# Kernel tuning notes

Hardware: AMD Instinct MI355X
Metric: run time of the kernel (lower is better)

Reference implementation:

```python
import jax, jax.numpy as jnp
import numpy as np

B, S, I = 64, 32, 64
N_ITEMS = 100000
E, H = 256, 128


def setup_inputs() -> dict:
    key = jax.random.key(0)
    k_len, k_ids, k_ut, k_emb, k_wih, k_whh, k_a1, k_a2, k_vt = jax.random.split(key, 9)
    n_sess = B * S
    # ragged session lengths in [2, I] -> trailing zero padding, all sessions valid
    lengths = jax.random.randint(k_len, (n_sess,), 2, I + 1)
    ids = jax.random.randint(k_ids, (n_sess, I), 1, N_ITEMS + 1)
    pad_mask = jnp.arange(I)[None, :] < lengths[:, None]
    item_id = (ids * pad_mask).reshape(B, S, I).astype(jnp.int32)
    eval_from = jnp.zeros((B,), dtype=jnp.int32)
    u_type = jax.random.randint(k_ut, (B,), 0, 5).astype(jnp.int32)
    sc = 0.05
    emb = jax.random.normal(k_emb, (N_ITEMS + 1, E), jnp.float32) * sc
    emb = emb.at[0].set(0.0)  # padding_idx=0
    W_ih = jax.random.normal(k_wih, (3 * H, E), jnp.float32) * sc
    W_hh = jax.random.normal(k_whh, (3 * H, H), jnp.float32) * sc
    b_ih = jnp.zeros((3 * H,), jnp.float32)
    b_hh = jnp.zeros((3 * H,), jnp.float32)
    W_a1 = jax.random.normal(k_a1, (H, H), jnp.float32) * sc
    W_a2 = jax.random.normal(k_a2, (H, H), jnp.float32) * sc
    W_vt = jax.random.normal(k_vt, (1, H), jnp.float32) * sc
    return {"item_id": item_id, "eval_from": eval_from, "u_type": u_type,
            "emb": emb, "W_ih": W_ih, "W_hh": W_hh, "b_ih": b_ih, "b_hh": b_hh,
            "W_a1": W_a1, "W_a2": W_a2, "W_vt": W_vt}


def _gru(x, lengths, W_ih, W_hh, b_ih, b_hh):
    # x: [L, N, E]; packed-GRU semantics: state frozen past each length,
    # outputs zero at padded steps (matches pad_packed_sequence).
    L, N, _ = x.shape
    Hh = W_hh.shape[1]

    def step(h, inp):
        xt, t = inp
        gi = xt @ W_ih.T + b_ih           # [N, 3H]
        gh = h @ W_hh.T + b_hh
        i_r, i_z, i_n = jnp.split(gi, 3, axis=-1)
        h_r, h_z, h_n = jnp.split(gh, 3, axis=-1)
        r = jax.nn.sigmoid(i_r + h_r)
        z = jax.nn.sigmoid(i_z + h_z)
        n = jnp.tanh(i_n + r * h_n)
        h_new = (1.0 - z) * n + z * h
        valid = (t < lengths)[:, None]
        h_next = jnp.where(valid, h_new, h)
        out = jnp.where(valid, h_new, 0.0)
        return h_next, out

    h0 = jnp.zeros((N, Hh), x.dtype)
    hT, outs = jax.lax.scan(step, h0, (x, jnp.arange(L)))
    return outs, hT  # outs: [L, N, H], hT: [N, H]


def reference(item_id, eval_from, u_type, emb, W_ih, W_hh, b_ih, b_hh, W_a1, W_a2, W_vt):
    b, s, i = item_id.shape
    ids = jnp.clip(item_id, 0)
    allow = jnp.arange(s)[None, :] >= eval_from[:, None]        # [B, S]
    ids = ids * allow[:, :, None].astype(ids.dtype)
    sess = ids.reshape(b * s, i)                                # [N, I]
    lengths = (sess != 0).sum(1)                                # all >= 2 by construction
    n = sess.shape[0]
    target = sess[jnp.arange(n), lengths - 1]
    len_in = lengths - 1
    L = i - 1  # static L_in_max; extra padded steps are masked out
    mask = (jnp.arange(L)[None, :] < len_in[:, None])           # [N, L]
    inp = sess[:, :L] * mask.astype(sess.dtype)
    x = emb[inp]                                                # [N, L, E] (dropout=identity, eval)
    outs, ht = _gru(x.transpose(1, 0, 2), len_in, W_ih, W_hh, b_ih, b_hh)
    gru = outs.transpose(1, 0, 2)                               # [N, L, H]
    q1 = jnp.einsum('nlh,kh->nlk', gru, W_a1)
    q2 = (ht @ W_a2.T)[:, None, :]
    alpha = jnp.einsum('nlh,oh->nlo', jax.nn.sigmoid(q1 + q2), W_vt)[..., 0] * mask
    c_loc = jnp.einsum('nl,nlh->nh', alpha, gru)
    reps = jnp.concatenate([c_loc, ht], axis=1)                 # [N, 2H] (ct dropout=identity)
    u = jnp.repeat(u_type, s)
    return reps, target, u
```

## Files before the change

kernel.cpp:

```cpp
#include <hip/hip_runtime.h>
#include <hip/hip_bf16.h>

#define NSESS 2048
#define NI 64
#define LL 63
#define EE 256
#define HH 128
#define GG 384

typedef __attribute__((ext_vector_type(8))) short short8;
typedef __attribute__((ext_vector_type(4))) float f32x4;

static __device__ __forceinline__ unsigned short f2b(float f) {
  union { float f; unsigned u; } v; v.f = f;
  unsigned r = (v.u + 0x7FFFu + ((v.u >> 16) & 1u)) >> 16;
  return (unsigned short)r;
}
static __device__ __forceinline__ float b2f(unsigned short s) {
  union { unsigned u; float f; } v; v.u = ((unsigned)s) << 16;
  return v.f;
}
static __device__ __forceinline__ float sigmoidf_(float x) {
  return 1.f / (1.f + __expf(-x));
}
static __device__ __forceinline__ float tanhf_(float x) {
  x = fminf(fmaxf(x, -15.f), 15.f);
  float e = __expf(-2.f * x);
  return (1.f - e) / (1.f + e);
}
static __device__ __forceinline__ void barrier_lds_only() {
  asm volatile("s_waitcnt lgkmcnt(0)" ::: "memory");
  __builtin_amdgcn_sched_barrier(0);
  __builtin_amdgcn_s_barrier();
  __builtin_amdgcn_sched_barrier(0);
}
static __device__ __forceinline__ void gload_lds16(const void* g, void* l) {
  __builtin_amdgcn_global_load_lds(
      (const __attribute__((address_space(1))) unsigned int*)g,
      (__attribute__((address_space(3))) unsigned int*)l, 16, 0, 0);
}

__global__ __launch_bounds__(64) void prep_kernel(const int* __restrict__ item_id,
                                                  const int* __restrict__ eval_from,
                                                  const int* __restrict__ u_type,
                                                  int* __restrict__ len_in,
                                                  int* __restrict__ inp,
                                                  float* __restrict__ out) {
  int n = blockIdx.x;
  int lane = threadIdx.x;
  int b = n >> 5, s = n & 31;
  int allow = (s >= eval_from[b]) ? 1 : 0;
  int id = item_id[n * NI + lane];
  if (id < 0) id = 0;
  id *= allow;
  unsigned long long m = __ballot(id != 0);
  int length = __popcll(m);
  int li = length - 1;
  int tv = __shfl(id, (length > 0) ? (length - 1) : 0, 64);
  int target = (length > 0) ? tv : 0;
  if (lane < LL) inp[n * LL + lane] = (lane < li) ? id : 0;
  if (lane == 0) {
    len_in[n] = li;
    out[NSESS * 256 + n] = (float)target;
    out[NSESS * 256 + NSESS + n] = (float)u_type[b];
  }
}

__global__ __launch_bounds__(256) void cvt_weights(const float* __restrict__ W_ih,
                                                   const float* __restrict__ W_hh,
                                                   const float* __restrict__ W_a1,
                                                   unsigned short* __restrict__ Wb,
                                                   unsigned short* __restrict__ Whs,
                                                   unsigned short* __restrict__ Wa1b) {
  int i = blockIdx.x * 256 + threadIdx.x;
  Wb[i] = f2b(W_ih[i]);
  if (i < GG * HH) Whs[i] = f2b(W_hh[i]);
  if (i < HH * HH) Wa1b[i] = f2b(W_a1[i]);
}

__global__ __launch_bounds__(512, 2) void gemm_in(const float* __restrict__ emb,
                                                  const unsigned short* __restrict__ Wb,
                                                  const float* __restrict__ b_ih,
                                                  const int* __restrict__ inp,
                                                  unsigned short* __restrict__ gi) {
  constexpr int XP = 264;
  __shared__ unsigned short Ash[2][16 * XP];

  const int t = threadIdx.x;
  const int lane = t & 63, w = t >> 6;
  const int ccol = lane & 15, kg = lane >> 4;
  const int g0 = w * 48;

  short8 bfr[3][8];
#pragma unroll
  for (int nt = 0; nt < 3; ++nt) {
    const unsigned short* wrow = Wb + (long)(g0 + nt * 16 + ccol) * EE + kg * 8;
#pragma unroll
    for (int c = 0; c < 8; ++c) bfr[nt][c] = *(const short8*)(wrow + c * 32);
  }
  float bias[3];
#pragma unroll
  for (int nt = 0; nt < 3; ++nt) bias[nt] = b_ih[g0 + nt * 16 + ccol];

  const int tile0 = blockIdx.x * 8;
  const int srow = t >> 5;
  const int scol = (t & 31) * 8;

  {
    long rid = inp[tile0 * 16 + srow];
    const float* x = emb + rid * EE + scol;
    float4 a0 = *(const float4*)x, a1 = *(const float4*)(x + 4);
    short8 v;
    v[0]=(short)f2b(a0.x); v[1]=(short)f2b(a0.y); v[2]=(short)f2b(a0.z); v[3]=(short)f2b(a0.w);
    v[4]=(short)f2b(a1.x); v[5]=(short)f2b(a1.y); v[6]=(short)f2b(a1.z); v[7]=(short)f2b(a1.w);
    *(short8*)(&Ash[0][srow * XP + scol]) = v;
  }
  __syncthreads();

  for (int i = 0; i < 8; ++i) {
    const int cur = i & 1;
    const int m0 = (tile0 + i) * 16;

    float4 a0, a1;
    if (i + 1 < 8) {
      long rid = inp[(tile0 + i + 1) * 16 + srow];
      const float* x = emb + rid * EE + scol;
      a0 = *(const float4*)x; a1 = *(const float4*)(x + 4);
    }

    f32x4 acc[3];
#pragma unroll
    for (int nt = 0; nt < 3; ++nt)
      acc[nt] = (f32x4){bias[nt], bias[nt], bias[nt], bias[nt]};
#pragma unroll
    for (int c = 0; c < 8; ++c) {
      short8 af = *(const short8*)(&Ash[cur][ccol * XP + c * 32 + kg * 8]);
#pragma unroll
      for (int nt = 0; nt < 3; ++nt)
        acc[nt] = __builtin_amdgcn_mfma_f32_16x16x32_bf16(af, bfr[nt][c], acc[nt], 0, 0, 0);
    }

    int nsd[4], lsd[4];
#pragma unroll
    for (int j = 0; j < 4; ++j) {
      int m = m0 + kg * 4 + j;
      nsd[j] = m / 63;
      lsd[j] = m - 63 * nsd[j];
    }
#pragma unroll
    for (int nt = 0; nt < 3; ++nt) {
      int g = g0 + nt * 16 + ccol;
#pragma unroll
      for (int j = 0; j < 4; ++j)
        gi[((long)lsd[j] * NSESS + nsd[j]) * GG + g] = f2b(acc[nt][j]);
    }

    if (i + 1 < 8) {
      short8 v;
      v[0]=(short)f2b(a0.x); v[1]=(short)f2b(a0.y); v[2]=(short)f2b(a0.z); v[3]=(short)f2b(a0.w);
      v[4]=(short)f2b(a1.x); v[5]=(short)f2b(a1.y); v[6]=(short)f2b(a1.z); v[7]=(short)f2b(a1.w);
      *(short8*)(&Ash[cur ^ 1][srow * XP + scol]) = v;
    }
    barrier_lds_only();
  }
}

__global__ __launch_bounds__(512) void gru_mfma(const unsigned short* __restrict__ Whs,
                                                const float* __restrict__ b_hh,
                                                const unsigned short* __restrict__ gi,
                                                const int* __restrict__ len_in,
                                                unsigned short* __restrict__ outs,
                                                float* __restrict__ ht,
                                                float* __restrict__ out) {
  __shared__ unsigned short Gbuf[2 * 12288];
  __shared__ unsigned short ring[2 * 2048];

  const int t = threadIdx.x;
  const int w = t >> 6, lane = t & 63;
  const int ccol = lane & 15, kg = lane >> 4;
  const int sbase = kg * 4;
  const int n0 = blockIdx.x * 16;
  const int jh = w * 16 + ccol;

  short8 bfr[3][4];
#pragma unroll
  for (int cls = 0; cls < 3; ++cls) {
    const unsigned short* wrow = Whs + (long)(cls * HH + jh) * HH;
#pragma unroll
    for (int c = 0; c < 4; ++c)
      bfr[cls][c] = *(const short8*)(wrow + c * 32 + kg * 8);
  }
  float bh[3];
#pragma unroll
  for (int cls = 0; cls < 3; ++cls) bh[cls] = b_hh[cls * HH + jh];

  int li[4];
#pragma unroll
  for (int r = 0; r < 4; ++r) li[r] = len_in[n0 + sbase + r];
  const int lin_d = len_in[n0 + (t >> 5)];
  float hold[4] = {0.f, 0.f, 0.f, 0.f};

  for (int idx = t; idx < 2 * 2048; idx += 512) ring[idx] = 0;

  auto do_stage = [&](int W2) {
    const int b = W2 & 1;
    const int l0s = W2 * 2;
#pragma unroll
    for (int i = 0; i < 3; ++i) {
      int u = i * 512 + t;
      int l2s = u / 768;
      int r1 = u - l2s * 768;
      int nn = r1 / 48;
      int seg = r1 - nn * 48;
      int lg = l0s + l2s; if (lg > 62) lg = 62;
      const unsigned short* gsrc = gi + ((long)lg * NSESS + n0 + nn) * GG + seg * 8;
      gload_lds16(gsrc, (char*)Gbuf + b * 24576 + u * 16);
    }
  };

  do_stage(0);
  do_stage(1);
  asm volatile("s_waitcnt vmcnt(3)" ::: "memory");
  __builtin_amdgcn_sched_barrier(0);
  barrier_lds_only();

  for (int W = 0; W < 32; ++W) {
    const int bsel = W & 1;
#pragma unroll
    for (int l2 = 0; l2 < 2; ++l2) {
      const int l = W * 2 + l2;
      if (l < LL) {
        const unsigned short* rb = ring + ((l + 1) & 1) * 2048 + ccol * HH;
        short8 af[4];
#pragma unroll
        for (int c = 0; c < 4; ++c)
          af[c] = *(const short8*)(rb + ((c * 32 + kg * 8) ^ ((ccol & 7) << 3)));

        const unsigned short* gb = Gbuf + bsel * 12288 + l2 * 6144;
        float gv[4][3];
#pragma unroll
        for (int r = 0; r < 4; ++r)
#pragma unroll
          for (int cls = 0; cls < 3; ++cls)
            gv[r][cls] = b2f(gb[(sbase + r) * GG + cls * HH + jh]);

        f32x4 acc[3];
#pragma unroll
        for (int cls = 0; cls < 3; ++cls) {
          acc[cls] = (f32x4){bh[cls], bh[cls], bh[cls], bh[cls]};
#pragma unroll
          for (int c = 0; c < 4; ++c)
            acc[cls] = __builtin_amdgcn_mfma_f32_16x16x32_bf16(af[c], bfr[cls][c], acc[cls], 0, 0, 0);
        }

        unsigned short* wrb = ring + (l & 1) * 2048;
#pragma unroll
        for (int r = 0; r < 4; ++r) {
          float rr = sigmoidf_(gv[r][0] + acc[0][r]);
          float zz = sigmoidf_(gv[r][1] + acc[1][r]);
          float nn = tanhf_(gv[r][2] + rr * acc[2][r]);
          float hnew = (1.f - zz) * nn + zz * hold[r];
          hold[r] = (l < li[r]) ? hnew : hold[r];
          int sess = sbase + r;
          wrb[sess * HH + (jh ^ ((sess & 7) << 3))] = f2b(hold[r]);
        }
        barrier_lds_only();
      }
    }

    {
      const int dn = t >> 5, dl2 = (t >> 4) & 1, dh = t & 15;
      const int dl = W * 2 + dl2;
      if (dl < LL) {
        short8 hv = *(const short8*)(ring + dl2 * 2048 + dn * HH + ((dh ^ (dn & 7)) << 3));
        if (dl >= lin_d) hv = (short8){0, 0, 0, 0, 0, 0, 0, 0};
        *(short8*)(outs + ((long)(n0 + dn) * LL + dl) * HH + dh * 8) = hv;
      }
    }
    if (W + 2 < 32) do_stage(W + 2);
    if (W < 30) {
      asm volatile("s_waitcnt vmcnt(4)" ::: "memory");
      __builtin_amdgcn_sched_barrier(0);
    } else if (W == 30) {
      asm volatile("s_waitcnt vmcnt(1)" ::: "memory");
      __builtin_amdgcn_sched_barrier(0);
    }
    if (W < 31) {
      __builtin_amdgcn_s_barrier();
      __builtin_amdgcn_sched_barrier(0);
    }
  }

#pragma unroll
  for (int r = 0; r < 4; ++r) {
    int n = n0 + sbase + r;
    ht[(long)n * HH + jh] = hold[r];
    out[(long)n * 256 + HH + jh] = hold[r];
  }
}

__global__ __launch_bounds__(256) void attn(const unsigned short* __restrict__ outs,
                                            const float* __restrict__ ht,
                                            const unsigned short* __restrict__ Wa1b,
                                            const float* __restrict__ W_a2,
                                            const float* __restrict__ W_vt,
                                            const int* __restrict__ len_in,
                                            float* __restrict__ out) {
  constexpr int OP = HH + 8;
  __shared__ unsigned short o_l[64 * OP];
  __shared__ float q2s[HH];
  __shared__ float wvt[HH];
  __shared__ float hts[HH];
  __shared__ float aw[4][64];
  __shared__ float alphas[64];

  const int n = blockIdx.x;
  const int t = threadIdx.x;
  const int lane = t & 63, wv = t >> 6;
  const int ccol = lane & 15, kg = lane >> 4;
  const int li = len_in[n];

  const unsigned* src = (const unsigned*)(outs + (long)n * LL * HH);
  for (int idx = t; idx < LL * 64; idx += 256) {
    int r = idx >> 6, c2 = idx & 63;
    ((unsigned*)(o_l + r * OP))[c2] = src[r * 64 + c2];
  }
  if (t < 64) ((unsigned*)(o_l + 63 * OP))[t] = 0;
  if (t < HH) { hts[t] = ht[(long)n * HH + t]; wvt[t] = W_vt[t]; }

  short8 bfr[2][4];
#pragma unroll
  for (int nt = 0; nt < 2; ++nt) {
    int G = wv * 32 + nt * 16 + ccol;
#pragma unroll
    for (int c = 0; c < 4; ++c)
      bfr[nt][c] = *(const short8*)(Wa1b + (long)G * HH + c * 32 + kg * 8);
  }
  __syncthreads();

  if (t < HH) {
    float a = 0.f;
    const float* w2 = W_a2 + t * HH;
    for (int k = 0; k < HH; ++k) a += hts[k] * w2[k];
    q2s[t] = a;
  }
  __syncthreads();

  f32x4 acc[4][2];
#pragma unroll
  for (int mt = 0; mt < 4; ++mt)
#pragma unroll
    for (int nt = 0; nt < 2; ++nt) acc[mt][nt] = (f32x4){0.f, 0.f, 0.f, 0.f};
#pragma unroll
  for (int mt = 0; mt < 4; ++mt) {
#pragma unroll
    for (int c = 0; c < 4; ++c) {
      short8 af = *(const short8*)(o_l + (mt * 16 + ccol) * OP + c * 32 + kg * 8);
#pragma unroll
      for (int nt = 0; nt < 2; ++nt)
        acc[mt][nt] = __builtin_amdgcn_mfma_f32_16x16x32_bf16(af, bfr[nt][c], acc[mt][nt], 0, 0, 0);
    }
  }

  float q2v[2], wvv[2];
#pragma unroll
  for (int nt = 0; nt < 2; ++nt) {
    int cg = wv * 32 + nt * 16 + ccol;
    q2v[nt] = q2s[cg]; wvv[nt] = wvt[cg];
  }
#pragma unroll
  for (int mt = 0; mt < 4; ++mt) {
    float part[4] = {0.f, 0.f, 0.f, 0.f};
#pragma unroll
    for (int nt = 0; nt < 2; ++nt)
#pragma unroll
      for (int j = 0; j < 4; ++j)
        part[j] += sigmoidf_(acc[mt][nt][j] + q2v[nt]) * wvv[nt];
#pragma unroll
    for (int j = 0; j < 4; ++j) {
#pragma unroll
      for (int off = 1; off < 16; off <<= 1)
        part[j] += __shfl_xor(part[j], off, 64);
    }
    if (ccol == 0) {
#pragma unroll
      for (int j = 0; j < 4; ++j) aw[wv][mt * 16 + kg * 4 + j] = part[j];
    }
  }
  __syncthreads();

  if (t < 64) {
    float s = aw[0][t] + aw[1][t] + aw[2][t] + aw[3][t];
    alphas[t] = (t < li) ? s : 0.f;
  }
  __syncthreads();

  if (t < HH) {
    float c = 0.f;
    for (int l = 0; l < LL; ++l) c = fmaf(alphas[l], b2f(o_l[l * OP + t]), c);
    out[(long)n * 256 + t] = c;
  }
}

extern "C" void kernel_launch(void* const* d_in, const int* in_sizes, int n_in,
                              void* d_out, int out_size, void* d_ws, size_t ws_size,
                              hipStream_t stream) {
  (void)in_sizes; (void)n_in; (void)out_size; (void)ws_size;
  const int* item_id   = (const int*)d_in[0];
  const int* eval_from = (const int*)d_in[1];
  const int* u_type    = (const int*)d_in[2];
  const float* emb     = (const float*)d_in[3];
  const float* W_ih    = (const float*)d_in[4];
  const float* W_hh    = (const float*)d_in[5];
  const float* b_ih    = (const float*)d_in[6];
  const float* b_hh    = (const float*)d_in[7];
  const float* W_a1    = (const float*)d_in[8];
  const float* W_a2    = (const float*)d_in[9];
  const float* W_vt    = (const float*)d_in[10];

  float* out = (float*)d_out;
  char* ws = (char*)d_ws;
  int* len_in           = (int*)(ws + 0);
  int* inp              = (int*)(ws + 8192);
  unsigned short* Wb    = (unsigned short*)(ws + 524288);
  unsigned short* Whs   = (unsigned short*)(ws + 720896);
  float* ht             = (float*)(ws + 819200);
  unsigned short* gi    = (unsigned short*)(ws + 1867776);
  unsigned short* outs  = (unsigned short*)(ws + 100958208);
  unsigned short* Wa1b  = (unsigned short*)(ws + 133988352);

  prep_kernel<<<NSESS, 64, 0, stream>>>(item_id, eval_from, u_type, len_in, inp, out);
  cvt_weights<<<384, 256, 0, stream>>>(W_ih, W_hh, W_a1, Wb, Whs, Wa1b);
  gemm_in<<<1008, 512, 0, stream>>>(emb, Wb, b_ih, inp, gi);
  gru_mfma<<<NSESS / 16, 512, 0, stream>>>(Whs, b_hh, gi, len_in, outs, ht, out);
  attn<<<NSESS, 512, 0, stream>>>(outs, ht, Wa1b, W_a2, W_vt, len_in, out);
}
```

Baseline: 159.5 us.

## Halve sessions per GRU block and reorder gate-input layout for vector loads

The GRU recurrence kernel now handles 8 sessions per block instead of 16, which doubles the grid to 256 blocks so more CUs share the serial recurrence. Half the MFMA rows in each step do no useful work. The input-gate buffer written by gemm_in is re-laid out per block of 8 sessions, so each thread reads its 4 gate values with a single 8-byte load, and the staging pipeline now covers 4 timesteps per stage. The tanh formula and the h update are also simplified, dropping the clamp and one multiply.

```diff
diff --git a/kernel.cpp b/kernel.cpp
--- a/kernel.cpp
+++ b/kernel.cpp
@@ -20,13 +20,18 @@
   union { unsigned u; float f; } v; v.u = ((unsigned)s) << 16;
   return v.f;
 }
+static __device__ __forceinline__ float lo16(unsigned u) {
+  union { unsigned v; float f; } x; x.v = u << 16; return x.f;
+}
+static __device__ __forceinline__ float hi16(unsigned u) {
+  union { unsigned v; float f; } x; x.v = u & 0xFFFF0000u; return x.f;
+}
 static __device__ __forceinline__ float sigmoidf_(float x) {
   return 1.f / (1.f + __expf(-x));
 }
-static __device__ __forceinline__ float tanhf_(float x) {
-  x = fminf(fmaxf(x, -15.f), 15.f);
-  float e = __expf(-2.f * x);
-  return (1.f - e) / (1.f + e);
+static __device__ __forceinline__ float tanh2_(float y) {
+  float e = __expf(2.f * y);
+  return 1.f - 2.f / (1.f + e);
 }
 static __device__ __forceinline__ void barrier_lds_only() {
   asm volatile("s_waitcnt lgkmcnt(0)" ::: "memory");
@@ -140,19 +145,21 @@
         acc[nt] = __builtin_amdgcn_mfma_f32_16x16x32_bf16(af, bfr[nt][c], acc[nt], 0, 0, 0);
     }
 
-    int nsd[4], lsd[4];
+    long base[4];
 #pragma unroll
     for (int j = 0; j < 4; ++j) {
       int m = m0 + kg * 4 + j;
-      nsd[j] = m / 63;
-      lsd[j] = m - 63 * nsd[j];
+      int n = m / 63;
+      int l = m - 63 * n;
+      base[j] = ((long)l * 256 + (n >> 3)) * 3072 + (n & 7);
     }
 #pragma unroll
     for (int nt = 0; nt < 3; ++nt) {
       int g = g0 + nt * 16 + ccol;
+      int go = (g >> 7) * 1024 + (g & 127) * 8;
 #pragma unroll
       for (int j = 0; j < 4; ++j)
-        gi[((long)lsd[j] * NSESS + nsd[j]) * GG + g] = f2b(acc[nt][j]);
+        gi[base[j] + go] = f2b(acc[nt][j]);
     }
 
     if (i + 1 < 8) {
@@ -173,14 +180,17 @@
                                                 float* __restrict__ ht,
                                                 float* __restrict__ out) {
   __shared__ unsigned short Gbuf[2 * 12288];
-  __shared__ unsigned short ring[2 * 2048];
+  __shared__ unsigned short ring[4 * 1024];
 
   const int t = threadIdx.x;
   const int w = t >> 6, lane = t & 63;
   const int ccol = lane & 15, kg = lane >> 4;
+  const int kge = kg & 1;
+  const bool act = kg < 2;
   const int sbase = kg * 4;
-  const int n0 = blockIdx.x * 16;
+  const int n0 = blockIdx.x * 8;
   const int jh = w * 16 + ccol;
+  const int rr = ccol & 7;
 
   short8 bfr[3][4];
 #pragma unroll
@@ -196,25 +206,24 @@
 
   int li[4];
 #pragma unroll
-  for (int r = 0; r < 4; ++r) li[r] = len_in[n0 + sbase + r];
-  const int lin_d = len_in[n0 + (t >> 5)];
+  for (int r = 0; r < 4; ++r) li[r] = act ? len_in[n0 + sbase + r] : 0;
   float hold[4] = {0.f, 0.f, 0.f, 0.f};
 
-  for (int idx = t; idx < 2 * 2048; idx += 512) ring[idx] = 0;
+  for (int idx = t; idx < 4096; idx += 512) ring[idx] = 0;
+
+  const int dl4 = t >> 7, dsess = (t >> 4) & 7, dcol = (t & 15) * 8;
+  const int dlen = len_in[n0 + dsess];
 
   auto do_stage = [&](int W2) {
     const int b = W2 & 1;
-    const int l0s = W2 * 2;
-#pragma unroll
-    for (int i = 0; i < 3; ++i) {
-      int u = i * 512 + t;
-      int l2s = u / 768;
-      int r1 = u - l2s * 768;
-      int nn = r1 / 48;
-      int seg = r1 - nn * 48;
-      int lg = l0s + l2s; if (lg > 62) lg = 62;
-      const unsigned short* gsrc = gi + ((long)lg * NSESS + n0 + nn) * GG + seg * 8;
-      gload_lds16(gsrc, (char*)Gbuf + b * 24576 + u * 16);
+#pragma unroll
+    for (int s = 0; s < 3; ++s) {
+      int u = s * 512 + t;
+      int ls = u / 384;
+      int off = (u - ls * 384) * 8;
+      int lg = 4 * W2 + ls; if (lg > 62) lg = 62;
+      const unsigned short* src = gi + ((long)lg * 256 + blockIdx.x) * 3072 + off;
+      gload_lds16(src, (char*)Gbuf + b * 24576 + u * 16);
     }
   };
 
@@ -224,25 +233,23 @@
   __builtin_amdgcn_sched_barrier(0);
   barrier_lds_only();
 
-  for (int W = 0; W < 32; ++W) {
-    const int bsel = W & 1;
-#pragma unroll
-    for (int l2 = 0; l2 < 2; ++l2) {
-      const int l = W * 2 + l2;
+  for (int W = 0; W < 16; ++W) {
+    const unsigned short* gb_base = Gbuf + (W & 1) * 12288;
+#pragma unroll
+    for (int l2 = 0; l2 < 4; ++l2) {
+      const int l = 4 * W + l2;
       if (l < LL) {
-        const unsigned short* rb = ring + ((l + 1) & 1) * 2048 + ccol * HH;
+        const unsigned short* rb = ring + ((l + 3) & 3) * 1024 + rr * HH;
         short8 af[4];
 #pragma unroll
         for (int c = 0; c < 4; ++c)
-          af[c] = *(const short8*)(rb + ((c * 32 + kg * 8) ^ ((ccol & 7) << 3)));
-
-        const unsigned short* gb = Gbuf + bsel * 12288 + l2 * 6144;
-        float gv[4][3];
-#pragma unroll
-        for (int r = 0; r < 4; ++r)
-#pragma unroll
-          for (int cls = 0; cls < 3; ++cls)
-            gv[r][cls] = b2f(gb[(sbase + r) * GG + cls * HH + jh]);
+          af[c] = *(const short8*)(rb + ((c * 32 + kg * 8) ^ (rr << 3)));
+
+        const unsigned short* gb = gb_base + l2 * 3072;
+        uint2 gp[3];
+#pragma unroll
+        for (int cls = 0; cls < 3; ++cls)
+          gp[cls] = *(const uint2*)(gb + cls * 1024 + jh * 8 + kge * 4);
 
         f32x4 acc[3];
 #pragma unroll
@@ -253,49 +260,56 @@
             acc[cls] = __builtin_amdgcn_mfma_f32_16x16x32_bf16(af[c], bfr[cls][c], acc[cls], 0, 0, 0);
         }
 
-        unsigned short* wrb = ring + (l & 1) * 2048;
-#pragma unroll
-        for (int r = 0; r < 4; ++r) {
-          float rr = sigmoidf_(gv[r][0] + acc[0][r]);
-          float zz = sigmoidf_(gv[r][1] + acc[1][r]);
-          float nn = tanhf_(gv[r][2] + rr * acc[2][r]);
-          float hnew = (1.f - zz) * nn + zz * hold[r];
-          hold[r] = (l < li[r]) ? hnew : hold[r];
-          int sess = sbase + r;
-          wrb[sess * HH + (jh ^ ((sess & 7) << 3))] = f2b(hold[r]);
+        if (act) {
+          float gvv[3][4];
+#pragma unroll
+          for (int cls = 0; cls < 3; ++cls) {
+            gvv[cls][0] = lo16(gp[cls].x); gvv[cls][1] = hi16(gp[cls].x);
+            gvv[cls][2] = lo16(gp[cls].y); gvv[cls][3] = hi16(gp[cls].y);
+          }
+          unsigned short* wrb = ring + (l & 3) * 1024;
+#pragma unroll
+          for (int r = 0; r < 4; ++r) {
+            float rg = sigmoidf_(gvv[0][r] + acc[0][r]);
+            float zg = sigmoidf_(gvv[1][r] + acc[1][r]);
+            float ng = tanh2_(gvv[2][r] + rg * acc[2][r]);
+            float hnew = ng + zg * (hold[r] - ng);
+            hold[r] = (l < li[r]) ? hnew : hold[r];
+            int sess = sbase + r;
+            wrb[sess * HH + (jh ^ (sess << 3))] = f2b(hold[r]);
+          }
         }
         barrier_lds_only();
       }
     }
 
     {
-      const int dn = t >> 5, dl2 = (t >> 4) & 1, dh = t & 15;
-      const int dl = W * 2 + dl2;
+      const int dl = 4 * W + dl4;
       if (dl < LL) {
-        short8 hv = *(const short8*)(ring + dl2 * 2048 + dn * HH + ((dh ^ (dn & 7)) << 3));
-        if (dl >= lin_d) hv = (short8){0, 0, 0, 0, 0, 0, 0, 0};
-        *(short8*)(outs + ((long)(n0 + dn) * LL + dl) * HH + dh * 8) = hv;
+        short8 hv = *(const short8*)(ring + dl4 * 1024 + dsess * HH + (dcol ^ (dsess << 3)));
+        if (dl >= dlen) hv = (short8){0, 0, 0, 0, 0, 0, 0, 0};
+        *(short8*)(outs + ((long)(n0 + dsess) * LL + dl) * HH + dcol) = hv;
       }
     }
-    if (W + 2 < 32) do_stage(W + 2);
-    if (W < 30) {
+    if (W + 2 < 16) do_stage(W + 2);
+    if (W < 14) {
       asm volatile("s_waitcnt vmcnt(4)" ::: "memory");
       __builtin_amdgcn_sched_barrier(0);
-    } else if (W == 30) {
+      barrier_lds_only();
+    } else if (W == 14) {
       asm volatile("s_waitcnt vmcnt(1)" ::: "memory");
       __builtin_amdgcn_sched_barrier(0);
-    }
-    if (W < 31) {
-      __builtin_amdgcn_s_barrier();
-      __builtin_amdgcn_sched_barrier(0);
-    }
-  }
-
-#pragma unroll
-  for (int r = 0; r < 4; ++r) {
-    int n = n0 + sbase + r;
-    ht[(long)n * HH + jh] = hold[r];
-    out[(long)n * 256 + HH + jh] = hold[r];
+      barrier_lds_only();
+    }
+  }
+
+  if (act) {
+#pragma unroll
+    for (int r = 0; r < 4; ++r) {
+      int n = n0 + sbase + r;
+      ht[(long)n * HH + jh] = hold[r];
+      out[(long)n * 256 + HH + jh] = hold[r];
+    }
   }
 }
 
@@ -432,6 +446,6 @@
   prep_kernel<<<NSESS, 64, 0, stream>>>(item_id, eval_from, u_type, len_in, inp, out);
   cvt_weights<<<384, 256, 0, stream>>>(W_ih, W_hh, W_a1, Wb, Whs, Wa1b);
   gemm_in<<<1008, 512, 0, stream>>>(emb, Wb, b_ih, inp, gi);
-  gru_mfma<<<NSESS / 16, 512, 0, stream>>>(Whs, b_hh, gi, len_in, outs, ht, out);
+  gru_mfma<<<NSESS / 8, 512, 0, stream>>>(Whs, b_hh, gi, len_in, outs, ht, out);
   attn<<<NSESS, 512, 0, stream>>>(outs, ht, Wa1b, W_a2, W_vt, len_in, out);
 }
```

Result: slower. 266.5 us (+67.0%).
